# Kernel tuning notes

Hardware: AMD Instinct MI355X
Metric: run time of the kernel (lower is better)

The kernel has to match this reference:

```python
import jax, jax.numpy as jnp
import numpy as np

# Model/config constants
N = 2048          # total nodes in batch
G = 32            # number of graphs
NPG = 64          # nodes per graph (N = G * NPG)
E = 16384         # total edges (E//G per graph, unique within graph)
HIDDEN = 256
N_HEADS = 8
HEAD_DIM = HIDDEN // N_HEADS
EDGE_FEAT = 16
SCALE = HEAD_DIM ** -0.5


def setup_inputs() -> dict:
    key = jax.random.key(0)
    ks = jax.random.split(key, 16)
    nodes = jax.random.normal(ks[0], (N, HIDDEN), dtype=jnp.float32)
    edges = jax.random.normal(ks[1], (E, EDGE_FEAT), dtype=jnp.float32)
    n_node = jnp.full((G,), NPG, dtype=jnp.int32)
    # Unique (sender, receiver) pairs within each graph block
    epg = E // G
    gkeys = jax.random.split(ks[2], G)
    perm = jax.vmap(lambda k: jax.random.permutation(k, NPG * NPG)[:epg])(gkeys)  # [G, epg]
    so = perm // NPG
    ro = perm % NPG
    base = (jnp.arange(G, dtype=jnp.int32) * NPG)[:, None]
    senders = (base + so).reshape(-1).astype(jnp.int32)
    receivers = (base + ro).reshape(-1).astype(jnp.int32)
    init = 0.02
    Wq = jax.random.normal(ks[3], (HIDDEN, HIDDEN), jnp.float32) * init
    Wk = jax.random.normal(ks[4], (HIDDEN, HIDDEN), jnp.float32) * init
    Wv = jax.random.normal(ks[5], (HIDDEN, HIDDEN), jnp.float32) * init
    Wo = jax.random.normal(ks[6], (HIDDEN, HIDDEN), jnp.float32) * init
    We = jax.random.normal(ks[7], (EDGE_FEAT, N_HEADS), jnp.float32) * init
    bq = jnp.zeros((HIDDEN,), jnp.float32)
    bk = jnp.zeros((HIDDEN,), jnp.float32)
    bv = jnp.zeros((HIDDEN,), jnp.float32)
    bo = jnp.zeros((HIDDEN,), jnp.float32)
    be = jnp.zeros((N_HEADS,), jnp.float32)
    return {"nodes": nodes, "edges": edges, "n_node": n_node,
            "senders": senders, "receivers": receivers,
            "Wq": Wq, "bq": bq, "Wk": Wk, "bk": bk, "Wv": Wv, "bv": bv,
            "Wo": Wo, "bo": bo, "We": We, "be": be}


def reference(nodes, edges, n_node, senders, receivers,
              Wq, bq, Wk, bk, Wv, bv, Wo, bo, We, be):
    n_nodes = nodes.shape[0]
    n_graphs = n_node.shape[0]
    q = (nodes @ Wq + bq).reshape(n_nodes, N_HEADS, HEAD_DIM)
    k = (nodes @ Wk + bk).reshape(n_nodes, N_HEADS, HEAD_DIM)
    v = (nodes @ Wv + bv).reshape(n_nodes, N_HEADS, HEAD_DIM)
    scores = jnp.einsum('ihd,jhd->ijh', q, k) * SCALE  # [N, N, H]
    graph_idx = jnp.repeat(jnp.arange(n_graphs), n_node, total_repeat_length=n_nodes)
    same_graph = graph_idx[:, None] == graph_idx[None, :]
    scores = scores + jnp.where(same_graph[:, :, None], 0.0, -1e9)
    # Edge bias scattered into [N, N, H] at (receiver, sender)
    edge_bias = edges @ We + be  # [E, H]
    edge_bias_matrix = jnp.zeros((n_nodes, n_nodes, N_HEADS), dtype=scores.dtype)
    edge_bias_matrix = edge_bias_matrix.at[receivers, senders].set(edge_bias)
    scores = scores + edge_bias_matrix
    attn = jax.nn.softmax(scores, axis=1)  # softmax over key axis j
    out = jnp.einsum('ijh,jhd->ihd', attn, v).reshape(n_nodes, HIDDEN)
    return out @ Wo + bo
```

## Files before the change

### kernel.cpp

```cpp
#include <hip/hip_runtime.h>

#define N_NODES 2048
#define N_GRAPHS 32
#define NPG 64
#define N_EDGES 16384
#define EPG 512
#define HIDDEN 256
#define NHEADS 8
#define HEADDIM 32
#define EDGEFEAT 16
#define ATT_SCALE 0.17677669529663687f

typedef unsigned short u16;
typedef __attribute__((ext_vector_type(8))) short bf16x8;
typedef __attribute__((ext_vector_type(4))) float f32x4;

__device__ __forceinline__ u16 f2b(float f) {
    unsigned x = __float_as_uint(f);
    return (u16)((x + 0x7fffu + ((x >> 16) & 1u)) >> 16);
}
__device__ __forceinline__ float b2f(u16 u) {
    return __uint_as_float(((unsigned)u) << 16);
}
__device__ __forceinline__ unsigned pack2(float a, float b) {
    return (unsigned)f2b(a) | ((unsigned)f2b(b) << 16);
}

__global__ __launch_bounds__(256)
void qkv_attn_fused(const float* __restrict__ nodes,
                    const float* __restrict__ Wq, const float* __restrict__ Wk,
                    const float* __restrict__ Wv,
                    const float* __restrict__ bq, const float* __restrict__ bk,
                    const float* __restrict__ bv,
                    const float* __restrict__ edges, const float* __restrict__ We,
                    const float* __restrict__ be,
                    const int* __restrict__ senders, const int* __restrict__ receivers,
                    u16* __restrict__ attnb)
{
    const int g = blockIdx.x, h = blockIdx.y;
    const int tid = threadIdx.x;
    const int lane = tid & 63, wv = tid >> 6;
    const int l16 = lane & 15, quad = lane >> 4;

    __shared__ __align__(16) unsigned char smem[84480];
    short* An = (short*)smem;
    short* Wt = (short*)smem + 64 * 264;
    short* qhi = (short*)smem;
    short* qlo = qhi + 64 * 40;
    short* khi = qlo + 64 * 40;
    short* klo = khi + 64 * 40;
    short* vsT = klo + 64 * 40;
    float* sc  = (float*)(smem + 25088);
    float* red = sc + 64 * 65;
    __shared__ float we_h[EDGEFEAT];
    __shared__ float sbe;

    if (tid < EDGEFEAT) we_h[tid] = We[tid * NHEADS + h];
    if (tid == 0) sbe = be[h];

    #pragma unroll
    for (int rep = 0; rep < 16; ++rep) {
        const int q = rep * 256 + tid;
        const int row = q >> 6, f4 = q & 63;
        float4 x = *(const float4*)(nodes + (size_t)(g * NPG + row) * HIDDEN + f4 * 4);
        *(uint2*)&An[row * 264 + f4 * 4] = make_uint2(pack2(x.x, x.y), pack2(x.z, x.w));
    }
    #pragma unroll
    for (int rep = 0; rep < 24; ++rep) {
        const int q = rep * 256 + tid;
        const float* Wp = (rep < 8) ? Wq : (rep < 16) ? Wk : Wv;
        const int r = q & 2047;
        const int krow = r >> 3, f4 = r & 7;
        float4 x = *(const float4*)(Wp + (size_t)krow * HIDDEN + h * HEADDIM + f4 * 4);
        const int nb = (rep >> 3) * 32 + f4 * 4;
        Wt[(nb + 0) * 264 + krow] = (short)f2b(x.x);
        Wt[(nb + 1) * 264 + krow] = (short)f2b(x.y);
        Wt[(nb + 2) * 264 + krow] = (short)f2b(x.z);
        Wt[(nb + 3) * 264 + krow] = (short)f2b(x.w);
    }
    __syncthreads();

    f32x4 acc[6];
    #pragma unroll
    for (int nt = 0; nt < 6; ++nt) acc[nt] = (f32x4){0.f, 0.f, 0.f, 0.f};
    const int arow = (wv * 16 + l16) * 264 + quad * 8;
    #pragma unroll
    for (int k0 = 0; k0 < HIDDEN; k0 += 32) {
        bf16x8 af = *(const bf16x8*)&An[arow + k0];
        #pragma unroll
        for (int nt = 0; nt < 6; ++nt) {
            bf16x8 bf = *(const bf16x8*)&Wt[(nt * 16 + l16) * 264 + k0 + quad * 8];
            acc[nt] = __builtin_amdgcn_mfma_f32_16x16x32_bf16(af, bf, acc[nt], 0, 0, 0);
        }
    }
    __syncthreads();

    #pragma unroll
    for (int nt = 0; nt < 6; ++nt) {
        const int tns = nt >> 1;
        const int col = (nt & 1) * 16 + l16;
        const float* bp = (tns == 0) ? bq : (tns == 1) ? bk : bv;
        const float bias = bp[h * HEADDIM + col];
        #pragma unroll
        for (int r = 0; r < 4; ++r) {
            const int row = wv * 16 + quad * 4 + r;
            const float val = acc[nt][r] + bias;
            if (tns == 2) {
                vsT[col * 72 + row] = (short)f2b(val);
            } else {
                const u16 hi = f2b(val);
                const u16 lo = f2b(val - b2f(hi));
                if (tns == 0) { qhi[row * 40 + col] = (short)hi; qlo[row * 40 + col] = (short)lo; }
                else          { khi[row * 40 + col] = (short)hi; klo[row * 40 + col] = (short)lo; }
            }
        }
    }
    __syncthreads();

    {
        bf16x8 qh = *(const bf16x8*)&qhi[(wv * 16 + l16) * 40 + quad * 8];
        bf16x8 ql = *(const bf16x8*)&qlo[(wv * 16 + l16) * 40 + quad * 8];
        #pragma unroll
        for (int nt = 0; nt < 4; ++nt) {
            bf16x8 kh = *(const bf16x8*)&khi[(nt * 16 + l16) * 40 + quad * 8];
            bf16x8 kl = *(const bf16x8*)&klo[(nt * 16 + l16) * 40 + quad * 8];
            f32x4 s = (f32x4){0.f, 0.f, 0.f, 0.f};
            s = __builtin_amdgcn_mfma_f32_16x16x32_bf16(qh, kh, s, 0, 0, 0);
            s = __builtin_amdgcn_mfma_f32_16x16x32_bf16(qh, kl, s, 0, 0, 0);
            s = __builtin_amdgcn_mfma_f32_16x16x32_bf16(ql, kh, s, 0, 0, 0);
            #pragma unroll
            for (int r = 0; r < 4; ++r)
                sc[(wv * 16 + quad * 4 + r) * 65 + nt * 16 + l16] = s[r] * ATT_SCALE;
        }
    }
    __syncthreads();

    #pragma unroll
    for (int rep = 0; rep < 2; ++rep) {
        const int e = g * EPG + rep * 256 + tid;
        const float* ef = edges + (size_t)e * EDGEFEAT;
        float4 f0 = *(const float4*)(ef + 0);
        float4 f1 = *(const float4*)(ef + 4);
        float4 f2 = *(const float4*)(ef + 8);
        float4 f3 = *(const float4*)(ef + 12);
        float b = sbe
            + f0.x * we_h[0]  + f0.y * we_h[1]  + f0.z * we_h[2]  + f0.w * we_h[3]
            + f1.x * we_h[4]  + f1.y * we_h[5]  + f1.z * we_h[6]  + f1.w * we_h[7]
            + f2.x * we_h[8]  + f2.y * we_h[9]  + f2.z * we_h[10] + f2.w * we_h[11]
            + f3.x * we_h[12] + f3.y * we_h[13] + f3.z * we_h[14] + f3.w * we_h[15];
        const int s_l = senders[e] & (NPG - 1);
        const int r_l = receivers[e] & (NPG - 1);
        sc[r_l * 65 + s_l] += b;
    }
    __syncthreads();

    {
        const int i  = tid & 63;
        const int cg = tid >> 6;
        float* red_m = red;
        float* red_s = red + 4 * 64;
        float m = -1e30f;
        #pragma unroll
        for (int jj = 0; jj < 16; ++jj) m = fmaxf(m, sc[i * 65 + cg * 16 + jj]);
        red_m[cg * 64 + i] = m;
        __syncthreads();
        m = fmaxf(fmaxf(red_m[0 * 64 + i], red_m[1 * 64 + i]),
                  fmaxf(red_m[2 * 64 + i], red_m[3 * 64 + i]));
        float s = 0.f;
        #pragma unroll
        for (int jj = 0; jj < 16; ++jj) {
            const int j = cg * 16 + jj;
            float e = __expf(sc[i * 65 + j] - m);
            sc[i * 65 + j] = e;
            s += e;
        }
        red_s[cg * 64 + i] = s;
        __syncthreads();
        const float inv = 1.f / (red_s[0 * 64 + i] + red_s[1 * 64 + i] +
                                 red_s[2 * 64 + i] + red_s[3 * 64 + i]);
        #pragma unroll
        for (int jj = 0; jj < 16; ++jj) sc[i * 65 + cg * 16 + jj] *= inv;
    }
    __syncthreads();

    {
        f32x4 oacc[2];
        oacc[0] = (f32x4){0.f, 0.f, 0.f, 0.f};
        oacc[1] = (f32x4){0.f, 0.f, 0.f, 0.f};
        #pragma unroll
        for (int k0 = 0; k0 < NPG; k0 += 32) {
            float p[8];
            #pragma unroll
            for (int jj = 0; jj < 8; ++jj)
                p[jj] = sc[(wv * 16 + l16) * 65 + k0 + quad * 8 + jj];
            uint4 uh, ul;
            u16 h0 = f2b(p[0]), h1 = f2b(p[1]), h2 = f2b(p[2]), h3 = f2b(p[3]);
            u16 h4 = f2b(p[4]), h5 = f2b(p[5]), h6 = f2b(p[6]), h7 = f2b(p[7]);
            uh.x = (unsigned)h0 | ((unsigned)h1 << 16);
            uh.y = (unsigned)h2 | ((unsigned)h3 << 16);
            uh.z = (unsigned)h4 | ((unsigned)h5 << 16);
            uh.w = (unsigned)h6 | ((unsigned)h7 << 16);
            ul.x = pack2(p[0] - b2f(h0), p[1] - b2f(h1));
            ul.y = pack2(p[2] - b2f(h2), p[3] - b2f(h3));
            ul.z = pack2(p[4] - b2f(h4), p[5] - b2f(h5));
            ul.w = pack2(p[6] - b2f(h6), p[7] - b2f(h7));
            bf16x8 ph = *(bf16x8*)&uh;
            bf16x8 pl = *(bf16x8*)&ul;
            #pragma unroll
            for (int nt = 0; nt < 2; ++nt) {
                bf16x8 vf = *(const bf16x8*)&vsT[(nt * 16 + l16) * 72 + k0 + quad * 8];
                oacc[nt] = __builtin_amdgcn_mfma_f32_16x16x32_bf16(ph, vf, oacc[nt], 0, 0, 0);
                oacc[nt] = __builtin_amdgcn_mfma_f32_16x16x32_bf16(pl, vf, oacc[nt], 0, 0, 0);
            }
        }
        #pragma unroll
        for (int nt = 0; nt < 2; ++nt) {
            const int d = nt * 16 + l16;
            #pragma unroll
            for (int r = 0; r < 4; ++r) {
                const int row = wv * 16 + quad * 4 + r;
                attnb[(size_t)(g * NPG + row) * HIDDEN + h * HEADDIM + d] =
                    f2b(oacc[nt][r]);
            }
        }
    }
}

__global__ __launch_bounds__(256)
void outproj_fused(const u16* __restrict__ A,
                   const float* __restrict__ Wo,
                   const float* __restrict__ bo,
                   float* __restrict__ C)
{
    const int n0 = blockIdx.x * 64, m0 = blockIdx.y * 64;
    const int tid = threadIdx.x;
    const int lane = tid & 63, wv = tid >> 6;
    const int l16 = lane & 15, quad = lane >> 4;

    __shared__ __align__(16) short Ab[64 * 264];
    __shared__ __align__(16) short Bb[64 * 264];

    #pragma unroll
    for (int rep = 0; rep < 8; ++rep) {
        const int q = rep * 256 + tid;
        const int row = q >> 5, u = q & 31;
        *(uint4*)&Ab[row * 264 + u * 8] =
            *(const uint4*)(A + (size_t)(m0 + row) * HIDDEN + u * 8);
    }
    #pragma unroll
    for (int rep = 0; rep < 16; ++rep) {
        const int q = rep * 256 + tid;
        const int f4 = q & 7;
        const int krow = (q >> 3) & 255;
        const int half = q >> 11;
        float4 x = *(const float4*)(Wo + (size_t)krow * HIDDEN + n0 + half * 32 + f4 * 4);
        const int nb = half * 32 + f4 * 4;
        Bb[(nb + 0) * 264 + krow] = (short)f2b(x.x);
        Bb[(nb + 1) * 264 + krow] = (short)f2b(x.y);
        Bb[(nb + 2) * 264 + krow] = (short)f2b(x.z);
        Bb[(nb + 3) * 264 + krow] = (short)f2b(x.w);
    }
    __syncthreads();

    f32x4 acc[4];
    #pragma unroll
    for (int nt = 0; nt < 4; ++nt) acc[nt] = (f32x4){0.f, 0.f, 0.f, 0.f};
    const int arow = (wv * 16 + l16) * 264 + quad * 8;
    #pragma unroll
    for (int k0 = 0; k0 < HIDDEN; k0 += 32) {
        bf16x8 af = *(const bf16x8*)&Ab[arow + k0];
        #pragma unroll
        for (int nt = 0; nt < 4; ++nt) {
            bf16x8 bf = *(const bf16x8*)&Bb[(nt * 16 + l16) * 264 + k0 + quad * 8];
            acc[nt] = __builtin_amdgcn_mfma_f32_16x16x32_bf16(af, bf, acc[nt], 0, 0, 0);
        }
    }

    #pragma unroll
    for (int nt = 0; nt < 4; ++nt) {
        const int col = n0 + nt * 16 + l16;
        const float bias = bo[col];
        #pragma unroll
        for (int r = 0; r < 4; ++r)
            C[(size_t)(m0 + wv * 16 + quad * 4 + r) * HIDDEN + col] = acc[nt][r] + bias;
    }
}

extern "C" void kernel_launch(void* const* d_in, const int* in_sizes, int n_in,
                              void* d_out, int out_size, void* d_ws, size_t ws_size,
                              hipStream_t stream)
{
    const float* nodes     = (const float*)d_in[0];
    const float* edges     = (const float*)d_in[1];
    const int*   senders   = (const int*)d_in[3];
    const int*   receivers = (const int*)d_in[4];
    const float* Wq = (const float*)d_in[5];
    const float* bq = (const float*)d_in[6];
    const float* Wk = (const float*)d_in[7];
    const float* bk = (const float*)d_in[8];
    const float* Wv = (const float*)d_in[9];
    const float* bv = (const float*)d_in[10];
    const float* Wo = (const float*)d_in[11];
    const float* bo = (const float*)d_in[12];
    const float* We = (const float*)d_in[13];
    const float* be = (const float*)d_in[14];
    float* out = (float*)d_out;

    u16* attnb = (u16*)d_ws;

    qkv_attn_fused<<<dim3(N_GRAPHS, NHEADS), dim3(256), 0, stream>>>(
        nodes, Wq, Wk, Wv, bq, bk, bv, edges, We, be, senders, receivers, attnb);
    outproj_fused<<<dim3(HIDDEN / 64, N_NODES / 64), dim3(256), 0, stream>>>(
        attnb, Wo, bo, out);
}
```

Baseline: 94.90 us.

## Precompute bf16 weights/edge bias in setup kernel; fuse out-projection via atomics

Adds a setup kernel that converts nodes and all four weight matrices to transposed bf16 in global memory, precomputes per-head edge biases with packed scatter indices, and zeroes the output. The attention kernel then reads bf16 operands straight from global memory for the QKV projection instead of staging converted tiles in LDS, cutting shared memory from about 84 KB to 44 KB. The out-projection is folded into the attention kernel, with each head block adding its partial product into the output through fp32 atomics, so the separate GEMM kernel is removed. The cost is atomic contention (eight heads per output element), nondeterministic summation order, and an extra pass that zeroes the output before accumulation.

```diff
diff --git a/kernel.cpp b/kernel.cpp
--- a/kernel.cpp
+++ b/kernel.cpp
@@ -27,84 +27,143 @@
 }
 
 __global__ __launch_bounds__(256)
-void qkv_attn_fused(const float* __restrict__ nodes,
-                    const float* __restrict__ Wq, const float* __restrict__ Wk,
-                    const float* __restrict__ Wv,
-                    const float* __restrict__ bq, const float* __restrict__ bk,
-                    const float* __restrict__ bv,
-                    const float* __restrict__ edges, const float* __restrict__ We,
-                    const float* __restrict__ be,
-                    const int* __restrict__ senders, const int* __restrict__ receivers,
-                    u16* __restrict__ attnb)
+void setup_pre(const float* __restrict__ nodes,
+               const float* __restrict__ Wq, const float* __restrict__ Wk,
+               const float* __restrict__ Wv, const float* __restrict__ Wo,
+               const float* __restrict__ edges, const float* __restrict__ We,
+               const float* __restrict__ be,
+               const int* __restrict__ senders, const int* __restrict__ receivers,
+               u16* __restrict__ nodesb,
+               u16* __restrict__ WT,
+               uint2* __restrict__ ebp,
+               float* __restrict__ out)
+{
+    const int b = blockIdx.x, tid = threadIdx.x;
+    __shared__ float sf[64 * 65];
+
+    if (b < 64) {
+        const int m = b >> 4, tile = b & 15;
+        const int k0 = (tile >> 2) * 64, n0 = (tile & 3) * 64;
+        const float* src = (m == 0) ? Wq : (m == 1) ? Wk : (m == 2) ? Wv : Wo;
+        u16* dst = WT + m * 65536;
+        #pragma unroll
+        for (int i = 0; i < 4; ++i) {
+            const int idx = i * 256 + tid, kr = idx >> 4, c4 = idx & 15;
+            float4 x = *(const float4*)(src + (size_t)(k0 + kr) * HIDDEN + n0 + c4 * 4);
+            sf[kr * 65 + c4 * 4 + 0] = x.x;
+            sf[kr * 65 + c4 * 4 + 1] = x.y;
+            sf[kr * 65 + c4 * 4 + 2] = x.z;
+            sf[kr * 65 + c4 * 4 + 3] = x.w;
+        }
+        __syncthreads();
+        #pragma unroll
+        for (int i = 0; i < 4; ++i) {
+            const int idx = i * 256 + tid, nr = idx >> 4, c4 = idx & 15;
+            uint2 w;
+            w.x = pack2(sf[(c4 * 4 + 0) * 65 + nr], sf[(c4 * 4 + 1) * 65 + nr]);
+            w.y = pack2(sf[(c4 * 4 + 2) * 65 + nr], sf[(c4 * 4 + 3) * 65 + nr]);
+            *(uint2*)&dst[(size_t)(n0 + nr) * HIDDEN + k0 + c4 * 4] = w;
+        }
+    } else if (b < 96) {
+        float* sWe = sf;
+        float* sbe = sf + 128;
+        if (tid < 128) sWe[tid] = We[tid];
+        if (tid < 8)  sbe[tid] = be[tid];
+        __syncthreads();
+        #pragma unroll
+        for (int it = 0; it < 2; ++it) {
+            const int e = (b - 64) * EPG + it * 256 + tid;
+            const float* ep = edges + (size_t)e * EDGEFEAT;
+            float4 f0 = *(const float4*)(ep + 0);
+            float4 f1 = *(const float4*)(ep + 4);
+            float4 f2 = *(const float4*)(ep + 8);
+            float4 f3 = *(const float4*)(ep + 12);
+            const float ef[16] = {f0.x, f0.y, f0.z, f0.w, f1.x, f1.y, f1.z, f1.w,
+                                  f2.x, f2.y, f2.z, f2.w, f3.x, f3.y, f3.z, f3.w};
+            const unsigned idx =
+                (unsigned)((receivers[e] & (NPG - 1)) * 65 + (senders[e] & (NPG - 1)));
+            #pragma unroll
+            for (int h = 0; h < NHEADS; ++h) {
+                float bias = sbe[h];
+                #pragma unroll
+                for (int f = 0; f < EDGEFEAT; ++f) bias += ef[f] * sWe[f * 8 + h];
+                ebp[(size_t)h * N_EDGES + e] = make_uint2(__float_as_uint(bias), idx);
+            }
+        }
+    } else if (b < 128) {
+        const int blk = b - 96;
+        #pragma unroll
+        for (int it = 0; it < 16; ++it) {
+            const int i = blk * 4096 + it * 256 + tid;
+            float4 x = ((const float4*)nodes)[i];
+            ((uint2*)nodesb)[i] = make_uint2(pack2(x.x, x.y), pack2(x.z, x.w));
+        }
+    } else {
+        const int blk = b - 128;
+        const float4 z = make_float4(0.f, 0.f, 0.f, 0.f);
+        #pragma unroll
+        for (int it = 0; it < 16; ++it)
+            ((float4*)out)[blk * 4096 + it * 256 + tid] = z;
+    }
+}
+
+__global__ __launch_bounds__(256)
+void attn_all(const u16* __restrict__ nodesb,
+              const u16* __restrict__ WT,
+              const float* __restrict__ bq, const float* __restrict__ bk,
+              const float* __restrict__ bv, const float* __restrict__ bo,
+              const uint2* __restrict__ ebp,
+              float* __restrict__ out)
 {
     const int g = blockIdx.x, h = blockIdx.y;
     const int tid = threadIdx.x;
-    const int lane = tid & 63, wv = tid >> 6;
+    const int lane = tid & 63, wvi = tid >> 6;
     const int l16 = lane & 15, quad = lane >> 4;
 
-    __shared__ __align__(16) unsigned char smem[84480];
-    short* An = (short*)smem;
-    short* Wt = (short*)smem + 64 * 264;
+    __shared__ __align__(16) unsigned char smem[43776];
     short* qhi = (short*)smem;
-    short* qlo = qhi + 64 * 40;
-    short* khi = qlo + 64 * 40;
-    short* klo = khi + 64 * 40;
-    short* vsT = klo + 64 * 40;
+    short* qlo = qhi + 2560;
+    short* khi = qlo + 2560;
+    short* klo = khi + 2560;
+    short* vsT = klo + 2560;
     float* sc  = (float*)(smem + 25088);
     float* red = sc + 64 * 65;
-    __shared__ float we_h[EDGEFEAT];
-    __shared__ float sbe;
-
-    if (tid < EDGEFEAT) we_h[tid] = We[tid * NHEADS + h];
-    if (tid == 0) sbe = be[h];
-
+
+    const uint2 e0 = ebp[(size_t)h * N_EDGES + g * EPG + tid];
+    const uint2 e1 = ebp[(size_t)h * N_EDGES + g * EPG + 256 + tid];
+    float biasv[6];
     #pragma unroll
-    for (int rep = 0; rep < 16; ++rep) {
-        const int q = rep * 256 + tid;
-        const int row = q >> 6, f4 = q & 63;
-        float4 x = *(const float4*)(nodes + (size_t)(g * NPG + row) * HIDDEN + f4 * 4);
-        *(uint2*)&An[row * 264 + f4 * 4] = make_uint2(pack2(x.x, x.y), pack2(x.z, x.w));
-    }
-    #pragma unroll
-    for (int rep = 0; rep < 24; ++rep) {
-        const int q = rep * 256 + tid;
-        const float* Wp = (rep < 8) ? Wq : (rep < 16) ? Wk : Wv;
-        const int r = q & 2047;
-        const int krow = r >> 3, f4 = r & 7;
-        float4 x = *(const float4*)(Wp + (size_t)krow * HIDDEN + h * HEADDIM + f4 * 4);
-        const int nb = (rep >> 3) * 32 + f4 * 4;
-        Wt[(nb + 0) * 264 + krow] = (short)f2b(x.x);
-        Wt[(nb + 1) * 264 + krow] = (short)f2b(x.y);
-        Wt[(nb + 2) * 264 + krow] = (short)f2b(x.z);
-        Wt[(nb + 3) * 264 + krow] = (short)f2b(x.w);
-    }
-    __syncthreads();
+    for (int nt = 0; nt < 6; ++nt) {
+        const int tns = nt >> 1;
+        const float* bp = (tns == 0) ? bq : (tns == 1) ? bk : bv;
+        biasv[nt] = bp[h * HEADDIM + (nt & 1) * 16 + l16];
+    }
 
     f32x4 acc[6];
     #pragma unroll
     for (int nt = 0; nt < 6; ++nt) acc[nt] = (f32x4){0.f, 0.f, 0.f, 0.f};
-    const int arow = (wv * 16 + l16) * 264 + quad * 8;
+    const u16* An = nodesb + (size_t)(g * NPG + wvi * 16 + l16) * HIDDEN + quad * 8;
     #pragma unroll
     for (int k0 = 0; k0 < HIDDEN; k0 += 32) {
-        bf16x8 af = *(const bf16x8*)&An[arow + k0];
+        bf16x8 af = *(const bf16x8*)(An + k0);
         #pragma unroll
         for (int nt = 0; nt < 6; ++nt) {
-            bf16x8 bf = *(const bf16x8*)&Wt[(nt * 16 + l16) * 264 + k0 + quad * 8];
-            acc[nt] = __builtin_amdgcn_mfma_f32_16x16x32_bf16(af, bf, acc[nt], 0, 0, 0);
-        }
-    }
-    __syncthreads();
+            const u16* bp = WT + (nt >> 1) * 65536
+                          + (size_t)(h * HEADDIM + (nt & 1) * 16 + l16) * HIDDEN
+                          + k0 + quad * 8;
+            acc[nt] = __builtin_amdgcn_mfma_f32_16x16x32_bf16(
+                af, *(const bf16x8*)bp, acc[nt], 0, 0, 0);
+        }
+    }
 
     #pragma unroll
     for (int nt = 0; nt < 6; ++nt) {
         const int tns = nt >> 1;
         const int col = (nt & 1) * 16 + l16;
-        const float* bp = (tns == 0) ? bq : (tns == 1) ? bk : bv;
-        const float bias = bp[h * HEADDIM + col];
         #pragma unroll
         for (int r = 0; r < 4; ++r) {
-            const int row = wv * 16 + quad * 4 + r;
-            const float val = acc[nt][r] + bias;
+            const int row = wvi * 16 + quad * 4 + r;
+            const float val = acc[nt][r] + biasv[nt];
             if (tns == 2) {
                 vsT[col * 72 + row] = (short)f2b(val);
             } else {
@@ -118,8 +177,8 @@
     __syncthreads();
 
     {
-        bf16x8 qh = *(const bf16x8*)&qhi[(wv * 16 + l16) * 40 + quad * 8];
-        bf16x8 ql = *(const bf16x8*)&qlo[(wv * 16 + l16) * 40 + quad * 8];
+        bf16x8 qh = *(const bf16x8*)&qhi[(wvi * 16 + l16) * 40 + quad * 8];
+        bf16x8 ql = *(const bf16x8*)&qlo[(wvi * 16 + l16) * 40 + quad * 8];
         #pragma unroll
         for (int nt = 0; nt < 4; ++nt) {
             bf16x8 kh = *(const bf16x8*)&khi[(nt * 16 + l16) * 40 + quad * 8];
@@ -130,28 +189,13 @@
             s = __builtin_amdgcn_mfma_f32_16x16x32_bf16(ql, kh, s, 0, 0, 0);
             #pragma unroll
             for (int r = 0; r < 4; ++r)
-                sc[(wv * 16 + quad * 4 + r) * 65 + nt * 16 + l16] = s[r] * ATT_SCALE;
-        }
-    }
-    __syncthreads();
-
-    #pragma unroll
-    for (int rep = 0; rep < 2; ++rep) {
-        const int e = g * EPG + rep * 256 + tid;
-        const float* ef = edges + (size_t)e * EDGEFEAT;
-        float4 f0 = *(const float4*)(ef + 0);
-        float4 f1 = *(const float4*)(ef + 4);
-        float4 f2 = *(const float4*)(ef + 8);
-        float4 f3 = *(const float4*)(ef + 12);
-        float b = sbe
-            + f0.x * we_h[0]  + f0.y * we_h[1]  + f0.z * we_h[2]  + f0.w * we_h[3]
-            + f1.x * we_h[4]  + f1.y * we_h[5]  + f1.z * we_h[6]  + f1.w * we_h[7]
-            + f2.x * we_h[8]  + f2.y * we_h[9]  + f2.z * we_h[10] + f2.w * we_h[11]
-            + f3.x * we_h[12] + f3.y * we_h[13] + f3.z * we_h[14] + f3.w * we_h[15];
-        const int s_l = senders[e] & (NPG - 1);
-        const int r_l = receivers[e] & (NPG - 1);
-        sc[r_l * 65 + s_l] += b;
-    }
+                sc[(wvi * 16 + quad * 4 + r) * 65 + nt * 16 + l16] = s[r] * ATT_SCALE;
+        }
+    }
+    __syncthreads();
+
+    sc[e0.y] += __uint_as_float(e0.x);
+    sc[e1.y] += __uint_as_float(e1.x);
     __syncthreads();
 
     {
@@ -192,7 +236,7 @@
             float p[8];
             #pragma unroll
             for (int jj = 0; jj < 8; ++jj)
-                p[jj] = sc[(wv * 16 + l16) * 65 + k0 + quad * 8 + jj];
+                p[jj] = sc[(wvi * 16 + l16) * 65 + k0 + quad * 8 + jj];
             uint4 uh, ul;
             u16 h0 = f2b(p[0]), h1 = f2b(p[1]), h2 = f2b(p[2]), h3 = f2b(p[3]);
             u16 h4 = f2b(p[4]), h5 = f2b(p[5]), h6 = f2b(p[6]), h7 = f2b(p[7]);
@@ -215,74 +259,30 @@
         }
         #pragma unroll
         for (int nt = 0; nt < 2; ++nt) {
-            const int d = nt * 16 + l16;
             #pragma unroll
             for (int r = 0; r < 4; ++r) {
-                const int row = wv * 16 + quad * 4 + r;
-                attnb[(size_t)(g * NPG + row) * HIDDEN + h * HEADDIM + d] =
-                    f2b(oacc[nt][r]);
+                const int row = wvi * 16 + quad * 4 + r;
+                qhi[row * 40 + nt * 16 + l16] = (short)f2b(oacc[nt][r]);
             }
         }
     }
-}
-
-__global__ __launch_bounds__(256)
-void outproj_fused(const u16* __restrict__ A,
-                   const float* __restrict__ Wo,
-                   const float* __restrict__ bo,
-                   float* __restrict__ C)
-{
-    const int n0 = blockIdx.x * 64, m0 = blockIdx.y * 64;
-    const int tid = threadIdx.x;
-    const int lane = tid & 63, wv = tid >> 6;
-    const int l16 = lane & 15, quad = lane >> 4;
-
-    __shared__ __align__(16) short Ab[64 * 264];
-    __shared__ __align__(16) short Bb[64 * 264];
-
-    #pragma unroll
-    for (int rep = 0; rep < 8; ++rep) {
-        const int q = rep * 256 + tid;
-        const int row = q >> 5, u = q & 31;
-        *(uint4*)&Ab[row * 264 + u * 8] =
-            *(const uint4*)(A + (size_t)(m0 + row) * HIDDEN + u * 8);
-    }
-    #pragma unroll
-    for (int rep = 0; rep < 16; ++rep) {
-        const int q = rep * 256 + tid;
-        const int f4 = q & 7;
-        const int krow = (q >> 3) & 255;
-        const int half = q >> 11;
-        float4 x = *(const float4*)(Wo + (size_t)krow * HIDDEN + n0 + half * 32 + f4 * 4);
-        const int nb = half * 32 + f4 * 4;
-        Bb[(nb + 0) * 264 + krow] = (short)f2b(x.x);
-        Bb[(nb + 1) * 264 + krow] = (short)f2b(x.y);
-        Bb[(nb + 2) * 264 + krow] = (short)f2b(x.z);
-        Bb[(nb + 3) * 264 + krow] = (short)f2b(x.w);
-    }
-    __syncthreads();
-
-    f32x4 acc[4];
-    #pragma unroll
-    for (int nt = 0; nt < 4; ++nt) acc[nt] = (f32x4){0.f, 0.f, 0.f, 0.f};
-    const int arow = (wv * 16 + l16) * 264 + quad * 8;
-    #pragma unroll
-    for (int k0 = 0; k0 < HIDDEN; k0 += 32) {
-        bf16x8 af = *(const bf16x8*)&Ab[arow + k0];
-        #pragma unroll
-        for (int nt = 0; nt < 4; ++nt) {
-            bf16x8 bf = *(const bf16x8*)&Bb[(nt * 16 + l16) * 264 + k0 + quad * 8];
-            acc[nt] = __builtin_amdgcn_mfma_f32_16x16x32_bf16(af, bf, acc[nt], 0, 0, 0);
-        }
-    }
-
-    #pragma unroll
-    for (int nt = 0; nt < 4; ++nt) {
-        const int col = n0 + nt * 16 + l16;
-        const float bias = bo[col];
-        #pragma unroll
-        for (int r = 0; r < 4; ++r)
-            C[(size_t)(m0 + wv * 16 + quad * 4 + r) * HIDDEN + col] = acc[nt][r] + bias;
+    __syncthreads();
+
+    {
+        bf16x8 afo = *(const bf16x8*)&qhi[(wvi * 16 + l16) * 40 + quad * 8];
+        const u16* WoT = WT + 3 * 65536;
+        #pragma unroll
+        for (int nt = 0; nt < 16; ++nt) {
+            const u16* bp = WoT + (size_t)(nt * 16 + l16) * HIDDEN + h * HEADDIM + quad * 8;
+            f32x4 c = __builtin_amdgcn_mfma_f32_16x16x32_bf16(
+                afo, *(const bf16x8*)bp, (f32x4){0.f, 0.f, 0.f, 0.f}, 0, 0, 0);
+            const float bn = (h == 0) ? bo[nt * 16 + l16] : 0.f;
+            #pragma unroll
+            for (int r = 0; r < 4; ++r)
+                atomicAdd(out + (size_t)(g * NPG + wvi * 16 + quad * 4 + r) * HIDDEN
+                              + nt * 16 + l16,
+                          c[r] + bn);
+        }
     }
 }
 
@@ -306,10 +306,13 @@
     const float* be = (const float*)d_in[14];
     float* out = (float*)d_out;
 
-    u16* attnb = (u16*)d_ws;
-
-    qkv_attn_fused<<<dim3(N_GRAPHS, NHEADS), dim3(256), 0, stream>>>(
-        nodes, Wq, Wk, Wv, bq, bk, bv, edges, We, be, senders, receivers, attnb);
-    outproj_fused<<<dim3(HIDDEN / 64, N_NODES / 64), dim3(256), 0, stream>>>(
-        attnb, Wo, bo, out);
-}
+    u16*   nodesb = (u16*)d_ws;
+    u16*   WT     = (u16*)((char*)d_ws + 1048576);
+    uint2* ebp    = (uint2*)((char*)d_ws + 1572864);
+
+    setup_pre<<<dim3(160), dim3(256), 0, stream>>>(
+        nodes, Wq, Wk, Wv, Wo, edges, We, be, senders, receivers,
+        nodesb, WT, ebp, out);
+    attn_all<<<dim3(N_GRAPHS, NHEADS), dim3(256), 0, stream>>>(
+        nodesb, WT, bq, bk, bv, bo, ebp, out);
+}
```

After: 113.1 us. +19.2%, slower.

## Pre-transpose Wo in extra blocks, simplify outproj to direct MFMA loads, prefetch edges

Applied to the files above, without the earlier changes.

Sixteen extra blocks are added to the attention kernel; they convert Wo to a transposed bf16 copy in workspace. This lets the out-projection kernel skip the LDS staging and per-block Wo conversion, loading MFMA operands straight from global memory with smaller 32x32 tiles across 512 blocks. Edge features and sender/receiver indices are loaded early in the attention kernel to hide their latency behind the QKV work. The trade-off is extra workspace traffic and uncoalesced 16-byte global operand loads in the GEMM.

```diff
diff --git a/kernel.cpp b/kernel.cpp
--- a/kernel.cpp
+++ b/kernel.cpp
@@ -29,16 +29,44 @@
 __global__ __launch_bounds__(256)
 void qkv_attn_fused(const float* __restrict__ nodes,
                     const float* __restrict__ Wq, const float* __restrict__ Wk,
-                    const float* __restrict__ Wv,
+                    const float* __restrict__ Wv, const float* __restrict__ Wo,
                     const float* __restrict__ bq, const float* __restrict__ bk,
                     const float* __restrict__ bv,
                     const float* __restrict__ edges, const float* __restrict__ We,
                     const float* __restrict__ be,
                     const int* __restrict__ senders, const int* __restrict__ receivers,
-                    u16* __restrict__ attnb)
+                    u16* __restrict__ attnb,
+                    u16* __restrict__ WoT)
 {
-    const int g = blockIdx.x, h = blockIdx.y;
+    const int bid = blockIdx.x;
     const int tid = threadIdx.x;
+
+    if (bid >= 256) {
+        __shared__ float sf[64 * 65];
+        const int tile = bid - 256;
+        const int k0 = (tile >> 2) * 64, n0 = (tile & 3) * 64;
+        #pragma unroll
+        for (int i = 0; i < 4; ++i) {
+            const int idx = i * 256 + tid, kr = idx >> 4, c4 = idx & 15;
+            float4 x = *(const float4*)(Wo + (size_t)(k0 + kr) * HIDDEN + n0 + c4 * 4);
+            sf[kr * 65 + c4 * 4 + 0] = x.x;
+            sf[kr * 65 + c4 * 4 + 1] = x.y;
+            sf[kr * 65 + c4 * 4 + 2] = x.z;
+            sf[kr * 65 + c4 * 4 + 3] = x.w;
+        }
+        __syncthreads();
+        #pragma unroll
+        for (int i = 0; i < 4; ++i) {
+            const int idx = i * 256 + tid, nr = idx >> 4, c4 = idx & 15;
+            uint2 w2;
+            w2.x = pack2(sf[(c4 * 4 + 0) * 65 + nr], sf[(c4 * 4 + 1) * 65 + nr]);
+            w2.y = pack2(sf[(c4 * 4 + 2) * 65 + nr], sf[(c4 * 4 + 3) * 65 + nr]);
+            *(uint2*)&WoT[(size_t)(n0 + nr) * HIDDEN + k0 + c4 * 4] = w2;
+        }
+        return;
+    }
+
+    const int g = bid >> 3, h = bid & 7;
     const int lane = tid & 63, wv = tid >> 6;
     const int l16 = lane & 15, quad = lane >> 4;
 
@@ -58,6 +86,23 @@
     if (tid < EDGEFEAT) we_h[tid] = We[tid * NHEADS + h];
     if (tid == 0) sbe = be[h];
 
+    const int e0i = g * EPG + tid;
+    const int e1i = e0i + 256;
+    const float* ep0 = edges + (size_t)e0i * EDGEFEAT;
+    const float* ep1 = edges + (size_t)e1i * EDGEFEAT;
+    const float4 a0 = *(const float4*)(ep0 + 0);
+    const float4 a1 = *(const float4*)(ep0 + 4);
+    const float4 a2 = *(const float4*)(ep0 + 8);
+    const float4 a3 = *(const float4*)(ep0 + 12);
+    const float4 c0 = *(const float4*)(ep1 + 0);
+    const float4 c1 = *(const float4*)(ep1 + 4);
+    const float4 c2 = *(const float4*)(ep1 + 8);
+    const float4 c3 = *(const float4*)(ep1 + 12);
+    const int s0 = senders[e0i] & (NPG - 1);
+    const int r0 = receivers[e0i] & (NPG - 1);
+    const int s1 = senders[e1i] & (NPG - 1);
+    const int r1 = receivers[e1i] & (NPG - 1);
+
     #pragma unroll
     for (int rep = 0; rep < 16; ++rep) {
         const int q = rep * 256 + tid;
@@ -135,22 +180,19 @@
     }
     __syncthreads();
 
-    #pragma unroll
-    for (int rep = 0; rep < 2; ++rep) {
-        const int e = g * EPG + rep * 256 + tid;
-        const float* ef = edges + (size_t)e * EDGEFEAT;
-        float4 f0 = *(const float4*)(ef + 0);
-        float4 f1 = *(const float4*)(ef + 4);
-        float4 f2 = *(const float4*)(ef + 8);
-        float4 f3 = *(const float4*)(ef + 12);
-        float b = sbe
-            + f0.x * we_h[0]  + f0.y * we_h[1]  + f0.z * we_h[2]  + f0.w * we_h[3]
-            + f1.x * we_h[4]  + f1.y * we_h[5]  + f1.z * we_h[6]  + f1.w * we_h[7]
-            + f2.x * we_h[8]  + f2.y * we_h[9]  + f2.z * we_h[10] + f2.w * we_h[11]
-            + f3.x * we_h[12] + f3.y * we_h[13] + f3.z * we_h[14] + f3.w * we_h[15];
-        const int s_l = senders[e] & (NPG - 1);
-        const int r_l = receivers[e] & (NPG - 1);
-        sc[r_l * 65 + s_l] += b;
+    {
+        const float b0 = sbe
+            + a0.x * we_h[0]  + a0.y * we_h[1]  + a0.z * we_h[2]  + a0.w * we_h[3]
+            + a1.x * we_h[4]  + a1.y * we_h[5]  + a1.z * we_h[6]  + a1.w * we_h[7]
+            + a2.x * we_h[8]  + a2.y * we_h[9]  + a2.z * we_h[10] + a2.w * we_h[11]
+            + a3.x * we_h[12] + a3.y * we_h[13] + a3.z * we_h[14] + a3.w * we_h[15];
+        sc[r0 * 65 + s0] += b0;
+        const float b1 = sbe
+            + c0.x * we_h[0]  + c0.y * we_h[1]  + c0.z * we_h[2]  + c0.w * we_h[3]
+            + c1.x * we_h[4]  + c1.y * we_h[5]  + c1.z * we_h[6]  + c1.w * we_h[7]
+            + c2.x * we_h[8]  + c2.y * we_h[9]  + c2.z * we_h[10] + c2.w * we_h[11]
+            + c3.x * we_h[12] + c3.y * we_h[13] + c3.z * we_h[14] + c3.w * we_h[15];
+        sc[r1 * 65 + s1] += b1;
     }
     __syncthreads();
 
@@ -227,63 +269,31 @@
 }
 
 __global__ __launch_bounds__(256)
-void outproj_fused(const u16* __restrict__ A,
-                   const float* __restrict__ Wo,
-                   const float* __restrict__ bo,
-                   float* __restrict__ C)
+void outproj(const u16* __restrict__ A,
+             const u16* __restrict__ WoT,
+             const float* __restrict__ bo,
+             float* __restrict__ C)
 {
-    const int n0 = blockIdx.x * 64, m0 = blockIdx.y * 64;
+    const int bid = blockIdx.x;
+    const int n0 = (bid & 7) * 32, m0 = (bid >> 3) * 32;
     const int tid = threadIdx.x;
-    const int lane = tid & 63, wv = tid >> 6;
+    const int lane = tid & 63, w = tid >> 6;
     const int l16 = lane & 15, quad = lane >> 4;
-
-    __shared__ __align__(16) short Ab[64 * 264];
-    __shared__ __align__(16) short Bb[64 * 264];
-
-    #pragma unroll
-    for (int rep = 0; rep < 8; ++rep) {
-        const int q = rep * 256 + tid;
-        const int row = q >> 5, u = q & 31;
-        *(uint4*)&Ab[row * 264 + u * 8] =
-            *(const uint4*)(A + (size_t)(m0 + row) * HIDDEN + u * 8);
-    }
-    #pragma unroll
-    for (int rep = 0; rep < 16; ++rep) {
-        const int q = rep * 256 + tid;
-        const int f4 = q & 7;
-        const int krow = (q >> 3) & 255;
-        const int half = q >> 11;
-        float4 x = *(const float4*)(Wo + (size_t)krow * HIDDEN + n0 + half * 32 + f4 * 4);
-        const int nb = half * 32 + f4 * 4;
-        Bb[(nb + 0) * 264 + krow] = (short)f2b(x.x);
-        Bb[(nb + 1) * 264 + krow] = (short)f2b(x.y);
-        Bb[(nb + 2) * 264 + krow] = (short)f2b(x.z);
-        Bb[(nb + 3) * 264 + krow] = (short)f2b(x.w);
-    }
-    __syncthreads();
-
-    f32x4 acc[4];
-    #pragma unroll
-    for (int nt = 0; nt < 4; ++nt) acc[nt] = (f32x4){0.f, 0.f, 0.f, 0.f};
-    const int arow = (wv * 16 + l16) * 264 + quad * 8;
+    const int mst = w & 1, nt = w >> 1;
+
+    f32x4 acc = (f32x4){0.f, 0.f, 0.f, 0.f};
+    const u16* Ar = A   + (size_t)(m0 + mst * 16 + l16) * HIDDEN + quad * 8;
+    const u16* Br = WoT + (size_t)(n0 + nt  * 16 + l16) * HIDDEN + quad * 8;
     #pragma unroll
     for (int k0 = 0; k0 < HIDDEN; k0 += 32) {
-        bf16x8 af = *(const bf16x8*)&Ab[arow + k0];
-        #pragma unroll
-        for (int nt = 0; nt < 4; ++nt) {
-            bf16x8 bf = *(const bf16x8*)&Bb[(nt * 16 + l16) * 264 + k0 + quad * 8];
-            acc[nt] = __builtin_amdgcn_mfma_f32_16x16x32_bf16(af, bf, acc[nt], 0, 0, 0);
-        }
-    }
-
-    #pragma unroll
-    for (int nt = 0; nt < 4; ++nt) {
-        const int col = n0 + nt * 16 + l16;
-        const float bias = bo[col];
-        #pragma unroll
-        for (int r = 0; r < 4; ++r)
-            C[(size_t)(m0 + wv * 16 + quad * 4 + r) * HIDDEN + col] = acc[nt][r] + bias;
-    }
+        acc = __builtin_amdgcn_mfma_f32_16x16x32_bf16(
+            *(const bf16x8*)(Ar + k0), *(const bf16x8*)(Br + k0), acc, 0, 0, 0);
+    }
+    const int col = n0 + nt * 16 + l16;
+    const float bias = bo[col];
+    #pragma unroll
+    for (int r = 0; r < 4; ++r)
+        C[(size_t)(m0 + mst * 16 + quad * 4 + r) * HIDDEN + col] = acc[r] + bias;
 }
 
 extern "C" void kernel_launch(void* const* d_in, const int* in_sizes, int n_in,
@@ -307,9 +317,11 @@
     float* out = (float*)d_out;
 
     u16* attnb = (u16*)d_ws;
-
-    qkv_attn_fused<<<dim3(N_GRAPHS, NHEADS), dim3(256), 0, stream>>>(
-        nodes, Wq, Wk, Wv, bq, bk, bv, edges, We, be, senders, receivers, attnb);
-    outproj_fused<<<dim3(HIDDEN / 64, N_NODES / 64), dim3(256), 0, stream>>>(
-        attnb, Wo, bo, out);
-}
+    u16* WoT   = (u16*)((char*)d_ws + 1048576);
+
+    qkv_attn_fused<<<dim3(272), dim3(256), 0, stream>>>(
+        nodes, Wq, Wk, Wv, Wo, bq, bk, bv, edges, We, be, senders, receivers,
+        attnb, WoT);
+    outproj<<<dim3(512), dim3(256), 0, stream>>>(
+        attnb, WoT, bo, out);
+}
```

Measured after the change: 98.30 us. 1.04x slower.
